# Performance work log

Hardware: AMD Instinct MI355X
Metric: run time of the kernel (lower is better)

The kernel has to match this reference:

```python
import jax, jax.numpy as jnp
import numpy as np
import math

DIM = 2048
N_HEADS = 16
HEAD_DIM = DIM // N_HEADS
B, S = 2, 2048
EPS = 1e-6


def rms_norm(x, w):
    return x * jax.lax.rsqrt(jnp.mean(x * x, axis=-1, keepdims=True) + EPS) * w


def rotate(x, cos, sin):
    x1, x2 = jnp.split(x, 2, axis=-1)
    rotated = jnp.concatenate((-x2, x1), axis=-1)
    return x * cos + rotated * sin


def setup_inputs() -> dict:
    key = jax.random.key(0)
    ks = jax.random.split(key, 16)
    half = HEAD_DIM // 2
    inv_freq = 1.0 / (10000.0 ** (jnp.arange(0, half, dtype=jnp.float32) / half))
    t = jnp.arange(S, dtype=jnp.float32)
    freqs = jnp.einsum('s,d->sd', t, inv_freq)
    emb = jnp.concatenate((freqs, freqs), axis=-1)  # [S, HEAD_DIM]
    cos = jnp.cos(emb)[None, None]  # [1,1,S,HEAD_DIM]
    sin = jnp.sin(emb)[None, None]
    # causal additive mask [1,1,S,S]
    causal = jnp.triu(jnp.full((S, S), -1e9, dtype=jnp.float32), k=1)[None, None]
    sc = 0.02
    return {
        'x': jax.random.normal(ks[0], (B, S, DIM), jnp.float32),
        'cos': cos,
        'sin': sin,
        'mask': causal,
        'attn_norm_w': jnp.ones((DIM,), jnp.float32),
        'ffn_norm_w': jnp.ones((DIM,), jnp.float32),
        'wq': jax.random.normal(ks[1], (DIM, DIM), jnp.float32) * sc,
        'wk': jax.random.normal(ks[2], (DIM, DIM), jnp.float32) * sc,
        'wv': jax.random.normal(ks[3], (DIM, DIM), jnp.float32) * sc,
        'wo': jax.random.normal(ks[4], (DIM, DIM), jnp.float32) * sc,
        'w1': jax.random.normal(ks[5], (DIM, 4 * DIM), jnp.float32) * sc,
        'w2': jax.random.normal(ks[6], (4 * DIM, DIM), jnp.float32) * sc,
        'w3': jax.random.normal(ks[7], (DIM, 4 * DIM), jnp.float32) * sc,
    }


def reference(x, cos, sin, mask, attn_norm_w, ffn_norm_w, wq, wk, wv, wo, w1, w2, w3):
    b, s, d = x.shape
    h = rms_norm(x, attn_norm_w)
    q = (h @ wq).reshape(b, s, N_HEADS, HEAD_DIM).transpose(0, 2, 1, 3)
    k = (h @ wk).reshape(b, s, N_HEADS, HEAD_DIM).transpose(0, 2, 1, 3)
    v = (h @ wv).reshape(b, s, N_HEADS, HEAD_DIM).transpose(0, 2, 1, 3)
    q = rotate(q, cos, sin)
    k = rotate(k, cos, sin)
    attn = jnp.einsum('bhqd,bhkd->bhqk', q, k) / math.sqrt(HEAD_DIM)
    attn = attn + mask
    attn = jax.nn.softmax(attn, axis=-1)
    out = jnp.einsum('bhqk,bhkd->bhqd', attn, v)
    out = out.transpose(0, 2, 1, 3).reshape(b, s, d)
    x = x + out @ wo
    h = rms_norm(x, ffn_norm_w)
    x = x + (jax.nn.silu(h @ w1) * (h @ w3)) @ w2
    return x
```

## Files before the change

kernel.cpp:

```cpp
#include <hip/hip_runtime.h>

#define DIM 2048
#define HDIM 128
#define NH 16
#define SEQ 2048
#define BATCH 2
#define MROWS (BATCH*SEQ)
#define QKP 6144

typedef __attribute__((ext_vector_type(8))) short short8;
typedef __attribute__((ext_vector_type(4))) float f32x4;

template<int N> struct ic { static constexpr int value = N; };

__device__ __forceinline__ unsigned short f2bf(float f) {
  union { float f; unsigned u; } v; v.f = f;
  unsigned r = v.u + 0x7FFFu + ((v.u >> 16) & 1u);
  return (unsigned short)(r >> 16);
}
__device__ __forceinline__ float bf2f(unsigned short b) {
  union { unsigned u; float f; } v; v.u = ((unsigned)b) << 16;
  return v.f;
}

__device__ __forceinline__ void gload16(const void* g, void* l) {
  __builtin_amdgcn_global_load_lds((const __attribute__((address_space(1))) unsigned int*)g,
                                   (__attribute__((address_space(3))) unsigned int*)l,
                                   16, 0, 0);
}

__global__ __launch_bounds__(256) void rmsnorm_kernel(const float* __restrict__ x,
                                                      const float* __restrict__ w,
                                                      unsigned short* __restrict__ out) {
  const int row = blockIdx.x;
  const int t = threadIdx.x;
  const float* xr = x + (size_t)row * DIM;
  float4 v0 = ((const float4*)xr)[t*2];
  float4 v1 = ((const float4*)xr)[t*2+1];
  float ss = v0.x*v0.x + v0.y*v0.y + v0.z*v0.z + v0.w*v0.w
           + v1.x*v1.x + v1.y*v1.y + v1.z*v1.z + v1.w*v1.w;
  #pragma unroll
  for (int i = 1; i < 64; i <<= 1) ss += __shfl_xor(ss, i);
  __shared__ float red[4];
  if ((t & 63) == 0) red[t >> 6] = ss;
  __syncthreads();
  float sum = red[0] + red[1] + red[2] + red[3];
  float sc = rsqrtf(sum * (1.0f/DIM) + 1e-6f);
  const float* wr = w + t*8;
  unsigned short ob[8];
  ob[0] = f2bf(v0.x*sc*wr[0]); ob[1] = f2bf(v0.y*sc*wr[1]);
  ob[2] = f2bf(v0.z*sc*wr[2]); ob[3] = f2bf(v0.w*sc*wr[3]);
  ob[4] = f2bf(v1.x*sc*wr[4]); ob[5] = f2bf(v1.y*sc*wr[5]);
  ob[6] = f2bf(v1.z*sc*wr[6]); ob[7] = f2bf(v1.w*sc*wr[7]);
  uint4 pk;
  pk.x = (unsigned)ob[0] | ((unsigned)ob[1] << 16);
  pk.y = (unsigned)ob[2] | ((unsigned)ob[3] << 16);
  pk.z = (unsigned)ob[4] | ((unsigned)ob[5] << 16);
  pk.w = (unsigned)ob[6] | ((unsigned)ob[7] << 16);
  *((uint4*)(out + (size_t)row*DIM + t*8)) = pk;
}

__global__ __launch_bounds__(256) void transpose3_kernel(const float* __restrict__ W0,
                                                         const float* __restrict__ W1,
                                                         const float* __restrict__ W2,
                                                         unsigned short* __restrict__ D0,
                                                         unsigned short* __restrict__ D1,
                                                         unsigned short* __restrict__ D2,
                                                         int K, int N) {
  const float* W = blockIdx.z == 0 ? W0 : (blockIdx.z == 1 ? W1 : W2);
  unsigned short* D = blockIdx.z == 0 ? D0 : (blockIdx.z == 1 ? D1 : D2);
  __shared__ float tile[64][65];
  const int k0 = blockIdx.x*64, n0 = blockIdx.y*64;
  const int t = threadIdx.x;
  const int rr = t >> 4, cc = (t & 15) * 4;
  #pragma unroll
  for (int i=0;i<4;i++) {
    float4 v = *(const float4*)&W[(size_t)(k0 + rr + i*16)*N + n0 + cc];
    tile[rr+i*16][cc] = v.x; tile[rr+i*16][cc+1] = v.y;
    tile[rr+i*16][cc+2] = v.z; tile[rr+i*16][cc+3] = v.w;
  }
  __syncthreads();
  #pragma unroll
  for (int j=0;j<4;j++) {
    const int n = rr + j*16;
    uint2 pk;
    pk.x = (unsigned)f2bf(tile[cc  ][n]) | ((unsigned)f2bf(tile[cc+1][n]) << 16);
    pk.y = (unsigned)f2bf(tile[cc+2][n]) | ((unsigned)f2bf(tile[cc+3][n]) << 16);
    *(uint2*)&D[(size_t)(n0 + n)*K + k0 + cc] = pk;
  }
}

__global__ __launch_bounds__(256) void transpose_v_kernel(const unsigned short* __restrict__ v,
                                                          int vpitch,
                                                          unsigned short* __restrict__ vt) {
  __shared__ unsigned short tile[32][33];
  const int b = blockIdx.z;
  const int s0 = blockIdx.x*32, c0 = blockIdx.y*32;
  const int tx = threadIdx.x & 31, ty = threadIdx.x >> 5;
  #pragma unroll
  for (int i=0;i<4;i++) tile[ty+i*8][tx] = v[((size_t)(b*SEQ + s0+ty+i*8))*vpitch + c0+tx];
  __syncthreads();
  #pragma unroll
  for (int i=0;i<4;i++) vt[((size_t)(b*DIM + c0+ty+i*8))*SEQ + s0+tx] = tile[tx][ty+i*8];
}

__global__ __launch_bounds__(256) void rope_qk(unsigned short* __restrict__ qk,
                                               const float* __restrict__ cosb,
                                               const float* __restrict__ sinb) {
  const size_t idx = (size_t)blockIdx.x * 256 + threadIdx.x;
  const int d = (int)(idx & 63);
  const int h = (int)((idx >> 6) & 31);
  const int row = (int)(idx >> 11);
  const int s = row & (SEQ-1);
  const size_t base = (size_t)row * QKP + h*HDIM + d;
  float a  = bf2f(qk[base]);
  float bq = bf2f(qk[base+64]);
  float c1 = cosb[s*HDIM + d],    s1 = sinb[s*HDIM + d];
  float c2 = cosb[s*HDIM + d+64], s2 = sinb[s*HDIM + d+64];
  qk[base]    = f2bf(a*c1 - bq*s1);
  qk[base+64] = f2bf(bq*c2 + a*s2);
}

template<int EPI>
__global__ __launch_bounds__(512, 2) void gemm_pipe32(const unsigned short* __restrict__ A,
                                                      const unsigned short* __restrict__ Bt,
                                                      const float* __restrict__ aux,
                                                      void* __restrict__ outp,
                                                      int M, int N, int K) {
  extern __shared__ unsigned short ldsd[];
  const int tid = threadIdx.x, l = tid & 63, wid = tid >> 6;
  const int wm = wid >> 2, wn = wid & 3;
  const int lr = l & 15, lg = l >> 4;
  const int bh = wn >> 1, brow0 = (wn & 1)*64;

  const int nbx = N >> 8;
  const int SW = (nbx >= 8) ? (nbx >> 3) : 1;
  const int xcd = (int)blockIdx.x & 7;
  const int ii  = (int)blockIdx.x >> 3;
  const int by = ii / SW;
  const int bx = xcd * SW + (ii % SW);
  const int m0 = by * 256, n0 = bx * 256;

  const int jks = ((lg ^ ((lr ^ (lr >> 2)) & 3)) << 3);
  const unsigned short* ldsA0 = ldsd + wm*4096 + lr*32 + jks;
  const unsigned short* ldsB0 = ldsd + 16384 + bh*4096 + brow0*32 + lr*32 + jks;

  const int srow = tid >> 2;
  const int jsw = (((tid & 3) ^ ((srow ^ (srow >> 2)) & 3)) << 3);
  const unsigned short* srcA[2];
  const unsigned short* srcB[2];
  #pragma unroll
  for (int h=0;h<2;h++) {
    srcA[h] = A  + (size_t)(m0 + h*128 + srow)*K + jsw;
    srcB[h] = Bt + (size_t)(n0 + h*128 + srow)*K + jsw;
  }
  unsigned short* dstL = ldsd + tid*8;

  int kO = 0;
  auto stA = [&](int db, int half, int tiled) {
    gload16(srcA[half] + kO + tiled, dstL + (db*2+half)*4096);
  };
  auto stB = [&](int db, int half, int tiled) {
    gload16(srcB[half] + kO + tiled, dstL + 16384 + (db*2+half)*4096);
  };

  f32x4 acc[8][4] = {};
  short8 bfrag[4];
  const int ntile = K >> 5;

  stB(0,0,0); stB(0,1,0);
  stA(0,0,0); stA(0,1,0);
  stB(1,0,32); stB(1,1,32);
  asm volatile("s_waitcnt vmcnt(2)" ::: "memory");
  __builtin_amdgcn_sched_barrier(0);
  __builtin_amdgcn_s_barrier();

  auto phase = [&](auto PC, auto LC) {
    constexpr int P = decltype(PC)::value;
    constexpr int LAST = decltype(LC)::value;
    constexpr int hi = P >> 2;
    constexpr int p  = P & 3;
    if constexpr (p == 0) {
      const unsigned short* bB = ldsB0 + hi*2*4096;
      #pragma unroll
      for (int nf=0;nf<4;nf++) bfrag[nf] = *(const short8*)(bB + nf*512);
    }
    const unsigned short* aB = ldsA0 + hi*2*4096;
    short8 afr[2];
    afr[0] = *(const short8*)(aB + (p*2  )*512);
    afr[1] = *(const short8*)(aB + (p*2+1)*512);
    if constexpr (P == 0)      stA(1, 0, 32);
    else if constexpr (P == 1) stA(1, 1, 32);
    else if constexpr (!LAST) {
      if constexpr (P == 2)      stB(0, 0, 64);
      else if constexpr (P == 3) stB(0, 1, 64);
      else if constexpr (P == 4) stA(0, 0, 64);
      else if constexpr (P == 5) stA(0, 1, 64);
      else if constexpr (P == 6) stB(1, 0, 96);
      else if constexpr (P == 7) stB(1, 1, 96);
    }
    if constexpr (P == 3) {
      if constexpr (LAST) { asm volatile("s_waitcnt vmcnt(0)" ::: "memory"); }
      else                { asm volatile("s_waitcnt vmcnt(2)" ::: "memory"); }
    }
    if constexpr (P == 7 && !LAST) {
      asm volatile("s_waitcnt vmcnt(2)" ::: "memory");
    }
    __builtin_amdgcn_s_barrier();
    asm volatile("s_waitcnt lgkmcnt(0)" ::: "memory");
    __builtin_amdgcn_sched_barrier(0);
    __builtin_amdgcn_s_setprio(1);
    #pragma unroll
    for (int mi=0;mi<2;mi++)
      #pragma unroll
      for (int nf=0;nf<4;nf++)
        acc[p*2+mi][nf] = __builtin_amdgcn_mfma_f32_16x16x32_bf16(afr[mi], bfrag[nf], acc[p*2+mi][nf], 0,0,0);
    __builtin_amdgcn_s_setprio(0);
    __builtin_amdgcn_s_barrier();
  };

  for (int T = 0; T + 2 < ntile; T += 2, kO += 64) {
    phase(ic<0>{}, ic<0>{}); phase(ic<1>{}, ic<0>{});
    phase(ic<2>{}, ic<0>{}); phase(ic<3>{}, ic<0>{});
    phase(ic<4>{}, ic<0>{}); phase(ic<5>{}, ic<0>{});
    phase(ic<6>{}, ic<0>{}); phase(ic<7>{}, ic<0>{});
  }
  phase(ic<0>{}, ic<1>{}); phase(ic<1>{}, ic<1>{});
  phase(ic<2>{}, ic<1>{}); phase(ic<3>{}, ic<1>{});
  phase(ic<4>{}, ic<1>{}); phase(ic<5>{}, ic<1>{});
  phase(ic<6>{}, ic<1>{}); phase(ic<7>{}, ic<1>{});

  #pragma unroll
  for (int mf = 0; mf < 8; mf++)
    #pragma unroll
    for (int nf = 0; nf < 4; nf++)
      #pragma unroll
      for (int r = 0; r < 4; r++) {
        const int row = m0 + wm*128 + mf*16 + lg*4 + r;
        const int col = n0 + wn*64 + nf*16 + lr;
        const size_t idx = (size_t)row * N + col;
        if constexpr (EPI == 0) {
          ((unsigned short*)outp)[idx] = f2bf(acc[mf][nf][r]);
        } else if constexpr (EPI == 1) {
          ((float*)outp)[idx] = acc[mf][nf][r] + aux[idx];
        } else {
          float g = acc[mf][nf][r];
          float u = bf2f(((unsigned short*)outp)[idx]);
          float sg = u / (1.0f + __expf(-u));
          ((unsigned short*)outp)[idx] = f2bf(sg * g);
        }
      }
}

template<int BM, int EPI>
__global__ __launch_bounds__(512, 2) void gemm_pipe(const unsigned short* __restrict__ A,
                                                    const unsigned short* __restrict__ Bt,
                                                    const float* __restrict__ aux,
                                                    void* __restrict__ outp,
                                                    int M, int N, int K) {
  constexpr int HRA = BM/2;
  constexpr int MF  = BM/32;
  constexpr int APP = MF/4;
  constexpr int LA  = BM/128;
  constexpr int AHS = HRA*64;
  constexpr int BB  = 4*AHS;
  extern __shared__ unsigned short ldsd[];
  const int tid = threadIdx.x, l = tid & 63, wid = tid >> 6;
  const int wm = wid >> 2, wn = wid & 3;
  const int lr = l & 15, lg = l >> 4;
  const int bh = wn >> 1, brow0 = (wn & 1)*64;

  const int nbx = N >> 8;
  const int SW = (nbx >= 8) ? (nbx >> 3) : 1;
  const int xcd = (int)blockIdx.x & 7;
  const int ii  = (int)blockIdx.x >> 3;
  const int by = ii / SW;
  const int bx = xcd * SW + (ii % SW);
  const int m0 = by * BM, n0 = bx * 256;

  const int m7 = lr & 7;
  const int jks0 = ((lg    ) ^ m7) << 3;
  const int jks1 = ((4 + lg) ^ m7) << 3;
  const unsigned short* ldsA0 = ldsd + wm*AHS + lr*64;
  const unsigned short* ldsA1 = ldsA0 + 2*AHS;
  const unsigned short* ldsB0 = ldsd + BB + bh*8192 + (brow0+lr)*64;
  const unsigned short* ldsB1 = ldsB0 + 2*8192;

  const int r0 = tid >> 3;
  const int jsw = ((tid & 7) ^ (r0 & 7)) << 3;
  const unsigned short* srcA[2][LA];
  #pragma unroll
  for (int h=0;h<2;h++)
    #pragma unroll
    for (int c=0;c<LA;c++)
      srcA[h][c] = A + (size_t)(m0 + h*HRA + c*64 + r0)*K + jsw;
  const unsigned short* srcB[2][2];
  #pragma unroll
  for (int h=0;h<2;h++)
    #pragma unroll
    for (int c=0;c<2;c++)
      srcB[h][c] = Bt + (size_t)(n0 + h*128 + c*64 + r0)*K + jsw;
  unsigned short* dstL = ldsd + tid*8;

  int kO = 0;
  auto stA = [&](int db, int half, int tiled) {
    #pragma unroll
    for (int c=0;c<LA;c++)
      gload16(srcA[half][c] + kO + tiled, dstL + (db*2+half)*AHS + c*4096);
  };
  auto stB = [&](int db, int half, int tiled) {
    #pragma unroll
    for (int c=0;c<2;c++)
      gload16(srcB[half][c] + kO + tiled, dstL + BB + (db*2+half)*8192 + c*4096);
  };

  f32x4 acc[MF][4] = {};
  short8 bfrag[4][2];
  const int ntile = K >> 6;

  stB(0,0,0); stB(0,1,0);
  stA(0,0,0); stA(0,1,0);
  stB(1,0,64); stB(1,1,64);
  asm volatile("s_waitcnt vmcnt(4)" ::: "memory");
  __builtin_amdgcn_sched_barrier(0);
  __builtin_amdgcn_s_barrier();

  auto phase = [&](auto PC, auto LC) {
    constexpr int P = decltype(PC)::value;
    constexpr int LAST = decltype(LC)::value;
    constexpr int hi = P >> 2;
    constexpr int p  = P & 3;
    if constexpr (p == 0) {
      const unsigned short* bB = hi ? ldsB1 : ldsB0;
      #pragma unroll
      for (int nf=0;nf<4;nf++) {
        bfrag[nf][0] = *(const short8*)(bB + nf*1024 + jks0);
        bfrag[nf][1] = *(const short8*)(bB + nf*1024 + jks1);
      }
    }
    const unsigned short* aB = hi ? ldsA1 : ldsA0;
    short8 afr[APP][2];
    #pragma unroll
    for (int mi=0;mi<APP;mi++) {
      afr[mi][0] = *(const short8*)(aB + (p*APP+mi)*1024 + jks0);
      afr[mi][1] = *(const short8*)(aB + (p*APP+mi)*1024 + jks1);
    }
    if constexpr (P == 0)      stA(1, 0, 64);
    else if constexpr (P == 1) stA(1, 1, 64);
    else if constexpr (!LAST) {
      if constexpr (P == 2)      stB(0, 0, 128);
      else if constexpr (P == 3) stB(0, 1, 128);
      else if constexpr (P == 4) stA(0, 0, 128);
      else if constexpr (P == 5) stA(0, 1, 128);
      else if constexpr (P == 6) stB(1, 0, 192);
      else if constexpr (P == 7) stB(1, 1, 192);
    }
    if constexpr (p == 0) {
      asm volatile("s_waitcnt lgkmcnt(8)" ::: "memory");
    }
    if constexpr (P == 3) {
      if constexpr (LAST) { asm volatile("s_waitcnt vmcnt(0)" ::: "memory"); }
      else                { asm volatile("s_waitcnt vmcnt(4)" ::: "memory"); }
    }
    if constexpr (P == 7 && !LAST) {
      asm volatile("s_waitcnt vmcnt(4)" ::: "memory");
    }
    __builtin_amdgcn_s_barrier();
    asm volatile("s_waitcnt lgkmcnt(0)" ::: "memory");
    __builtin_amdgcn_sched_barrier(0);
    __builtin_amdgcn_s_setprio(1);
    #pragma unroll
    for (int mi=0;mi<APP;mi++)
      #pragma unroll
      for (int nf=0;nf<4;nf++)
        #pragma unroll
        for (int ks=0;ks<2;ks++)
          acc[p*APP+mi][nf] = __builtin_amdgcn_mfma_f32_16x16x32_bf16(afr[mi][ks], bfrag[nf][ks], acc[p*APP+mi][nf], 0,0,0);
    __builtin_amdgcn_s_setprio(0);
    __builtin_amdgcn_s_barrier();
  };

  for (int T = 0; T + 2 < ntile; T += 2, kO += 128) {
    phase(ic<0>{}, ic<0>{}); phase(ic<1>{}, ic<0>{});
    phase(ic<2>{}, ic<0>{}); phase(ic<3>{}, ic<0>{});
    phase(ic<4>{}, ic<0>{}); phase(ic<5>{}, ic<0>{});
    phase(ic<6>{}, ic<0>{}); phase(ic<7>{}, ic<0>{});
  }
  phase(ic<0>{}, ic<1>{}); phase(ic<1>{}, ic<1>{});
  phase(ic<2>{}, ic<1>{}); phase(ic<3>{}, ic<1>{});
  phase(ic<4>{}, ic<1>{}); phase(ic<5>{}, ic<1>{});
  phase(ic<6>{}, ic<1>{}); phase(ic<7>{}, ic<1>{});

  #pragma unroll
  for (int mf = 0; mf < MF; mf++)
    #pragma unroll
    for (int nf = 0; nf < 4; nf++)
      #pragma unroll
      for (int r = 0; r < 4; r++) {
        const int row = m0 + wm*HRA + mf*16 + lg*4 + r;
        const int col = n0 + wn*64 + nf*16 + lr;
        const size_t idx = (size_t)row * N + col;
        if constexpr (EPI == 0) {
          ((unsigned short*)outp)[idx] = f2bf(acc[mf][nf][r]);
        } else if constexpr (EPI == 1) {
          ((float*)outp)[idx] = acc[mf][nf][r] + aux[idx];
        } else {
          float g = acc[mf][nf][r];
          float u = bf2f(((unsigned short*)outp)[idx]);
          float sg = u / (1.0f + __expf(-u));
          ((unsigned short*)outp)[idx] = f2bf(sg * g);
        }
      }
}

__global__ __launch_bounds__(256, 2) void attn_kernel(const unsigned short* __restrict__ q,
                                                      const unsigned short* __restrict__ k,
                                                      const unsigned short* __restrict__ vt,
                                                      unsigned short* __restrict__ ao) {
  const int t = threadIdx.x, lane = t & 63, w = t >> 6;
  const int qt = (int)gridDim.x - 1 - (int)blockIdx.x;
  const int bh = blockIdx.y;
  const int b = bh >> 4, h = bh & 15;
  const int lr = lane & 15, lg = lane >> 4;
  const int q0w = qt*128 + w*32;

  __shared__ __attribute__((aligned(16))) unsigned short Kb[64*128];
  __shared__ __attribute__((aligned(16))) unsigned short Vb[128*64];
  __shared__ __attribute__((aligned(16))) unsigned short Ones[16*72];
  __shared__ __attribute__((aligned(16))) unsigned short P[4][32*72];
  unsigned short* pw = &P[w][0];

  for (int idx = t; idx < 16*72; idx += 256) Ones[idx] = (idx < 72) ? 0x3F80 : 0;

  short8 aq[2][4];
  {
    const unsigned short* qp = q + ((size_t)(b*SEQ + q0w + lr))*QKP + h*HDIM;
    #pragma unroll
    for (int mf=0;mf<2;mf++)
      #pragma unroll
      for (int c=0;c<4;c++) aq[mf][c] = *(const short8*)(qp + (size_t)mf*16*QKP + c*32 + lg*8);
  }

  f32x4 accO[2][8] = {};
  f32x4 accO9[2] = {};
  float mrow[2][4];
  #pragma unroll
  for (int mf=0;mf<2;mf++)
    #pragma unroll
    for (int r=0;r<4;r++) mrow[mf][r] = -3.0e38f;

  const float scale = 0.08838834764831845f;
  const unsigned short* kg = k + (size_t)(b*SEQ)*QKP + h*HDIM;
  const unsigned short* vg = vt + (size_t)(bh*HDIM)*SEQ;

  const unsigned short* kga[4]; const unsigned short* vga[4];
  unsigned short* kld[4]; unsigned short* vld[4];
  #pragma unroll
  for (int i=0;i<4;i++) {
    const int D = i*256 + t;
    const int rk = D >> 4, jk = D & 15;
    kga[i] = kg + (size_t)rk*QKP + ((jk ^ (rk & 7)) * 8);
    const int rv = D >> 3, jv = D & 7;
    vga[i] = vg + (size_t)rv*SEQ + ((jv ^ (rv & 7)) * 8);
    kld[i] = &Kb[i*2048 + w*512];
    vld[i] = &Vb[i*2048 + w*512];
  }

  const int KV_END = qt*128 + 128;

  for (int kv0 = 0; kv0 < KV_END; kv0 += 64) {
    #pragma unroll
    for (int i=0;i<4;i++) gload16(kga[i] + (size_t)kv0*QKP, kld[i]);
    #pragma unroll
    for (int i=0;i<4;i++) gload16(vga[i] + kv0, vld[i]);
    __syncthreads();

    if (kv0 < q0w + 32) {
      f32x4 sc[2][4] = {};
      #pragma unroll
      for (int blk=0;blk<4;blk++) {
        const int krow = blk*16 + lr;
        const int sw = (krow & 7) << 3;
        #pragma unroll
        for (int c=0;c<4;c++) {
          short8 bk = *(const short8*)&Kb[krow*128 + ((c*32 + lg*8) ^ sw)];
          sc[0][blk] = __builtin_amdgcn_mfma_f32_16x16x32_bf16(aq[0][c], bk, sc[0][blk], 0,0,0);
          sc[1][blk] = __builtin_amdgcn_mfma_f32_16x16x32_bf16(aq[1][c], bk, sc[1][blk], 0,0,0);
        }
      }
      #pragma unroll
      for (int mf=0;mf<2;mf++)
        #pragma unroll
        for (int blk=0;blk<4;blk++)
          #pragma unroll
          for (int r=0;r<4;r++) sc[mf][blk][r] *= scale;
      if (kv0 + 63 > q0w) {
        #pragma unroll
        for (int mf=0;mf<2;mf++)
          #pragma unroll
          for (int blk=0;blk<4;blk++)
            #pragma unroll
            for (int r=0;r<4;r++)
              if (kv0 + blk*16 + lr > q0w + mf*16 + lg*4 + r) sc[mf][blk][r] = -1.0e30f;
      }
      float pm[2][4];
      #pragma unroll
      for (int mf=0;mf<2;mf++)
        #pragma unroll
        for (int r=0;r<4;r++) {
          float m0 = fmaxf(fmaxf(sc[mf][0][r], sc[mf][1][r]), fmaxf(sc[mf][2][r], sc[mf][3][r]));
          #pragma unroll
          for (int x=1;x<16;x<<=1) m0 = fmaxf(m0, __shfl_xor(m0, x));
          pm[mf][r] = m0;
        }
      int need = 0;
      #pragma unroll
      for (int mf=0;mf<2;mf++)
        #pragma unroll
        for (int r=0;r<4;r++) need |= (pm[mf][r] > mrow[mf][r] + 8.0f) ? 1 : 0;
      if (__any(need)) {
        #pragma unroll
        for (int mf=0;mf<2;mf++)
          #pragma unroll
          for (int r=0;r<4;r++) {
            const float mn = fmaxf(mrow[mf][r], pm[mf][r]);
            const float fc = __expf(mrow[mf][r] - mn);
            mrow[mf][r] = mn;
            #pragma unroll
            for (int n=0;n<8;n++) accO[mf][n][r] *= fc;
            accO9[mf][r] *= fc;
          }
      }
      #pragma unroll
      for (int mf=0;mf<2;mf++)
        #pragma unroll
        for (int blk=0;blk<4;blk++)
          #pragma unroll
          for (int r=0;r<4;r++) {
            const float p = __expf(sc[mf][blk][r] - mrow[mf][r]);
            pw[(mf*16 + lg*4 + r)*72 + blk*16 + lr] = f2bf(p);
          }
      short8 ap[2][2];
      #pragma unroll
      for (int mf=0;mf<2;mf++)
        #pragma unroll
        for (int ks=0;ks<2;ks++) ap[mf][ks] = *(const short8*)&pw[(mf*16 + lr)*72 + ks*32 + lg*8];
      #pragma unroll
      for (int n=0;n<8;n++) {
        #pragma unroll
        for (int ks=0;ks<2;ks++) {
          const int vrow = n*16 + lr;
          const int sw = (vrow & 7) << 3;
          short8 bv = *(const short8*)&Vb[vrow*64 + ((ks*32 + lg*8) ^ sw)];
          accO[0][n] = __builtin_amdgcn_mfma_f32_16x16x32_bf16(ap[0][ks], bv, accO[0][n], 0,0,0);
          accO[1][n] = __builtin_amdgcn_mfma_f32_16x16x32_bf16(ap[1][ks], bv, accO[1][n], 0,0,0);
        }
      }
      #pragma unroll
      for (int ks=0;ks<2;ks++) {
        short8 bv9 = *(const short8*)&Ones[lr*72 + ks*32 + lg*8];
        accO9[0] = __builtin_amdgcn_mfma_f32_16x16x32_bf16(ap[0][ks], bv9, accO9[0], 0,0,0);
        accO9[1] = __builtin_amdgcn_mfma_f32_16x16x32_bf16(ap[1][ks], bv9, accO9[1], 0,0,0);
      }
    }
    __syncthreads();
  }

  #pragma unroll
  for (int mf=0;mf<2;mf++)
    #pragma unroll
    for (int r=0;r<4;r++) {
      const float lv = __shfl(accO9[mf][r], lane & 48);
      const float inv = 1.0f / lv;
      const size_t row = (size_t)(b*SEQ + q0w + mf*16 + lg*4 + r);
      #pragma unroll
      for (int n=0;n<8;n++)
        ao[row*DIM + h*HDIM + n*16 + lr] = f2bf(accO[mf][n][r] * inv);
    }
}

extern "C" void kernel_launch(void* const* d_in, const int* in_sizes, int n_in,
                              void* d_out, int out_size, void* d_ws, size_t ws_size,
                              hipStream_t stream) {
  (void)in_sizes; (void)n_in; (void)out_size; (void)ws_size;
  const float* x    = (const float*)d_in[0];
  const float* cosb = (const float*)d_in[1];
  const float* sinb = (const float*)d_in[2];
  const float* anw  = (const float*)d_in[4];
  const float* fnw  = (const float*)d_in[5];
  const float* wq   = (const float*)d_in[6];
  const float* wk   = (const float*)d_in[7];
  const float* wv   = (const float*)d_in[8];
  const float* wo   = (const float*)d_in[9];
  const float* w1   = (const float*)d_in[10];
  const float* w2   = (const float*)d_in[11];
  const float* w3   = (const float*)d_in[12];

  char* ws = (char*)d_ws;
  const size_t MB = 1048576;
  unsigned short* h     = (unsigned short*)(ws);
  unsigned short* qkvb  = (unsigned short*)(ws + 16*MB);
  unsigned short* mid   = qkvb;
  unsigned short* aob   = (unsigned short*)(ws + 67*MB);
  char* wt              = ws + 84*MB;
  unsigned short* wqkvT = (unsigned short*)wt;
  unsigned short* vtb   = (unsigned short*)wt;
  unsigned short* woT   = (unsigned short*)wt;
  unsigned short* w1T   = (unsigned short*)wt;
  unsigned short* w3T   = (unsigned short*)(wt + 32*MB);
  unsigned short* w2T   = (unsigned short*)wt;
  float* x1f = (float*)d_out;

  dim3 b256(256);
  constexpr unsigned LDS32 = 65536;
  constexpr unsigned LDS128 = 98304;

  rmsnorm_kernel<<<dim3(MROWS), b256, 0, stream>>>(x, anw, h);

  transpose3_kernel<<<dim3(32,32,3), b256, 0, stream>>>(wq, wk, wv,
      wqkvT, wqkvT + 4194304, wqkvT + 8388608, 2048, 2048);

  gemm_pipe32<0><<<dim3(384), dim3(512), LDS32, stream>>>(h, wqkvT, nullptr, qkvb, MROWS, 6144, 2048);

  rope_qk<<<dim3(32768), b256, 0, stream>>>(qkvb, cosb, sinb);

  transpose_v_kernel<<<dim3(64,64,2), b256, 0, stream>>>(qkvb + 4096, QKP, vtb);

  attn_kernel<<<dim3(16,32), b256, 0, stream>>>(qkvb, qkvb + 2048, vtb, aob);

  transpose3_kernel<<<dim3(32,32,1), b256, 0, stream>>>(wo, nullptr, nullptr,
      woT, nullptr, nullptr, 2048, 2048);
  gemm_pipe<128,1><<<dim3(256), dim3(512), LDS128, stream>>>(aob, woT, x, x1f, MROWS, 2048, 2048);

  rmsnorm_kernel<<<dim3(MROWS), b256, 0, stream>>>(x1f, fnw, h);

  transpose3_kernel<<<dim3(32,128,2), b256, 0, stream>>>(w1, w3, nullptr,
      w1T, w3T, nullptr, 2048, 8192);
  gemm_pipe32<0><<<dim3(512), dim3(512), LDS32, stream>>>(h, w1T, nullptr, mid, MROWS, 8192, 2048);
  gemm_pipe32<3><<<dim3(512), dim3(512), LDS32, stream>>>(h, w3T, nullptr, mid, MROWS, 8192, 2048);

  transpose3_kernel<<<dim3(128,32,1), b256, 0, stream>>>(w2, nullptr, nullptr,
      w2T, nullptr, nullptr, 8192, 2048);
  gemm_pipe<128,1><<<dim3(256), dim3(512), LDS128, stream>>>(mid, w2T, x1f, (float*)d_out, MROWS, 2048, 8192);
}
```

Baseline: 850.9 us.

## Fuse W1/W3 FFN GEMMs into dual-B kernel and use BK64 GEMM for QKV

Replaces the two separate gate/up GEMMs with a single kernel that loads each A tile once and multiplies it against both W1 and W3 tiles, then applies SiLU-times-gate in registers before writing. This avoids a second pass over the activations and the bf16 round-trip of the intermediate gate output. The QKV projection also switches from the 32-wide-K kernel to the existing 128-row gemm_pipe variant with more blocks. The dual kernel needs 160 KB of LDS and two accumulator sets, which likely limits it to one block per CU and raises register pressure.

```diff
diff --git a/kernel.cpp b/kernel.cpp
--- a/kernel.cpp
+++ b/kernel.cpp
@@ -121,137 +121,6 @@
   qk[base+64] = f2bf(bq*c2 + a*s2);
 }
 
-template<int EPI>
-__global__ __launch_bounds__(512, 2) void gemm_pipe32(const unsigned short* __restrict__ A,
-                                                      const unsigned short* __restrict__ Bt,
-                                                      const float* __restrict__ aux,
-                                                      void* __restrict__ outp,
-                                                      int M, int N, int K) {
-  extern __shared__ unsigned short ldsd[];
-  const int tid = threadIdx.x, l = tid & 63, wid = tid >> 6;
-  const int wm = wid >> 2, wn = wid & 3;
-  const int lr = l & 15, lg = l >> 4;
-  const int bh = wn >> 1, brow0 = (wn & 1)*64;
-
-  const int nbx = N >> 8;
-  const int SW = (nbx >= 8) ? (nbx >> 3) : 1;
-  const int xcd = (int)blockIdx.x & 7;
-  const int ii  = (int)blockIdx.x >> 3;
-  const int by = ii / SW;
-  const int bx = xcd * SW + (ii % SW);
-  const int m0 = by * 256, n0 = bx * 256;
-
-  const int jks = ((lg ^ ((lr ^ (lr >> 2)) & 3)) << 3);
-  const unsigned short* ldsA0 = ldsd + wm*4096 + lr*32 + jks;
-  const unsigned short* ldsB0 = ldsd + 16384 + bh*4096 + brow0*32 + lr*32 + jks;
-
-  const int srow = tid >> 2;
-  const int jsw = (((tid & 3) ^ ((srow ^ (srow >> 2)) & 3)) << 3);
-  const unsigned short* srcA[2];
-  const unsigned short* srcB[2];
-  #pragma unroll
-  for (int h=0;h<2;h++) {
-    srcA[h] = A  + (size_t)(m0 + h*128 + srow)*K + jsw;
-    srcB[h] = Bt + (size_t)(n0 + h*128 + srow)*K + jsw;
-  }
-  unsigned short* dstL = ldsd + tid*8;
-
-  int kO = 0;
-  auto stA = [&](int db, int half, int tiled) {
-    gload16(srcA[half] + kO + tiled, dstL + (db*2+half)*4096);
-  };
-  auto stB = [&](int db, int half, int tiled) {
-    gload16(srcB[half] + kO + tiled, dstL + 16384 + (db*2+half)*4096);
-  };
-
-  f32x4 acc[8][4] = {};
-  short8 bfrag[4];
-  const int ntile = K >> 5;
-
-  stB(0,0,0); stB(0,1,0);
-  stA(0,0,0); stA(0,1,0);
-  stB(1,0,32); stB(1,1,32);
-  asm volatile("s_waitcnt vmcnt(2)" ::: "memory");
-  __builtin_amdgcn_sched_barrier(0);
-  __builtin_amdgcn_s_barrier();
-
-  auto phase = [&](auto PC, auto LC) {
-    constexpr int P = decltype(PC)::value;
-    constexpr int LAST = decltype(LC)::value;
-    constexpr int hi = P >> 2;
-    constexpr int p  = P & 3;
-    if constexpr (p == 0) {
-      const unsigned short* bB = ldsB0 + hi*2*4096;
-      #pragma unroll
-      for (int nf=0;nf<4;nf++) bfrag[nf] = *(const short8*)(bB + nf*512);
-    }
-    const unsigned short* aB = ldsA0 + hi*2*4096;
-    short8 afr[2];
-    afr[0] = *(const short8*)(aB + (p*2  )*512);
-    afr[1] = *(const short8*)(aB + (p*2+1)*512);
-    if constexpr (P == 0)      stA(1, 0, 32);
-    else if constexpr (P == 1) stA(1, 1, 32);
-    else if constexpr (!LAST) {
-      if constexpr (P == 2)      stB(0, 0, 64);
-      else if constexpr (P == 3) stB(0, 1, 64);
-      else if constexpr (P == 4) stA(0, 0, 64);
-      else if constexpr (P == 5) stA(0, 1, 64);
-      else if constexpr (P == 6) stB(1, 0, 96);
-      else if constexpr (P == 7) stB(1, 1, 96);
-    }
-    if constexpr (P == 3) {
-      if constexpr (LAST) { asm volatile("s_waitcnt vmcnt(0)" ::: "memory"); }
-      else                { asm volatile("s_waitcnt vmcnt(2)" ::: "memory"); }
-    }
-    if constexpr (P == 7 && !LAST) {
-      asm volatile("s_waitcnt vmcnt(2)" ::: "memory");
-    }
-    __builtin_amdgcn_s_barrier();
-    asm volatile("s_waitcnt lgkmcnt(0)" ::: "memory");
-    __builtin_amdgcn_sched_barrier(0);
-    __builtin_amdgcn_s_setprio(1);
-    #pragma unroll
-    for (int mi=0;mi<2;mi++)
-      #pragma unroll
-      for (int nf=0;nf<4;nf++)
-        acc[p*2+mi][nf] = __builtin_amdgcn_mfma_f32_16x16x32_bf16(afr[mi], bfrag[nf], acc[p*2+mi][nf], 0,0,0);
-    __builtin_amdgcn_s_setprio(0);
-    __builtin_amdgcn_s_barrier();
-  };
-
-  for (int T = 0; T + 2 < ntile; T += 2, kO += 64) {
-    phase(ic<0>{}, ic<0>{}); phase(ic<1>{}, ic<0>{});
-    phase(ic<2>{}, ic<0>{}); phase(ic<3>{}, ic<0>{});
-    phase(ic<4>{}, ic<0>{}); phase(ic<5>{}, ic<0>{});
-    phase(ic<6>{}, ic<0>{}); phase(ic<7>{}, ic<0>{});
-  }
-  phase(ic<0>{}, ic<1>{}); phase(ic<1>{}, ic<1>{});
-  phase(ic<2>{}, ic<1>{}); phase(ic<3>{}, ic<1>{});
-  phase(ic<4>{}, ic<1>{}); phase(ic<5>{}, ic<1>{});
-  phase(ic<6>{}, ic<1>{}); phase(ic<7>{}, ic<1>{});
-
-  #pragma unroll
-  for (int mf = 0; mf < 8; mf++)
-    #pragma unroll
-    for (int nf = 0; nf < 4; nf++)
-      #pragma unroll
-      for (int r = 0; r < 4; r++) {
-        const int row = m0 + wm*128 + mf*16 + lg*4 + r;
-        const int col = n0 + wn*64 + nf*16 + lr;
-        const size_t idx = (size_t)row * N + col;
-        if constexpr (EPI == 0) {
-          ((unsigned short*)outp)[idx] = f2bf(acc[mf][nf][r]);
-        } else if constexpr (EPI == 1) {
-          ((float*)outp)[idx] = acc[mf][nf][r] + aux[idx];
-        } else {
-          float g = acc[mf][nf][r];
-          float u = bf2f(((unsigned short*)outp)[idx]);
-          float sg = u / (1.0f + __expf(-u));
-          ((unsigned short*)outp)[idx] = f2bf(sg * g);
-        }
-      }
-}
-
 template<int BM, int EPI>
 __global__ __launch_bounds__(512, 2) void gemm_pipe(const unsigned short* __restrict__ A,
                                                     const unsigned short* __restrict__ Bt,
@@ -413,6 +282,157 @@
       }
 }
 
+__global__ __launch_bounds__(512, 2) void gemm_dual(const unsigned short* __restrict__ A,
+                                                    const unsigned short* __restrict__ B1t,
+                                                    const unsigned short* __restrict__ B3t,
+                                                    unsigned short* __restrict__ outp,
+                                                    int M, int N, int K) {
+  constexpr int AHS = 4096;
+  constexpr int BB1 = 16384;
+  constexpr int BB3 = 49152;
+  extern __shared__ unsigned short ldsd[];
+  const int tid = threadIdx.x, l = tid & 63, wid = tid >> 6;
+  const int wm = wid >> 2, wn = wid & 3;
+  const int lr = l & 15, lg = l >> 4;
+  const int bh = wn >> 1, brow0 = (wn & 1)*64;
+
+  const int nbx = N >> 8;
+  const int SW = nbx >> 3;
+  const int xcd = (int)blockIdx.x & 7;
+  const int ii  = (int)blockIdx.x >> 3;
+  const int by = ii / SW;
+  const int bx = xcd * SW + (ii % SW);
+  const int m0 = by * 128, n0 = bx * 256;
+
+  const int m7 = lr & 7;
+  const int jks0 = ((lg    ) ^ m7) << 3;
+  const int jks1 = ((4 + lg) ^ m7) << 3;
+  const unsigned short* ldsA0 = ldsd + wm*AHS + lr*64;
+  const unsigned short* ldsB1_ = ldsd + BB1 + bh*8192 + (brow0+lr)*64;
+  const unsigned short* ldsB3_ = ldsd + BB3 + bh*8192 + (brow0+lr)*64;
+
+  const int r0 = tid >> 3;
+  const int jsw = ((tid & 7) ^ (r0 & 7)) << 3;
+  const unsigned short* srcA[2];
+  #pragma unroll
+  for (int h=0;h<2;h++) srcA[h] = A + (size_t)(m0 + h*64 + r0)*K + jsw;
+  const unsigned short* srcB1[2][2];
+  const unsigned short* srcB3[2][2];
+  #pragma unroll
+  for (int h=0;h<2;h++)
+    #pragma unroll
+    for (int c=0;c<2;c++) {
+      srcB1[h][c] = B1t + (size_t)(n0 + h*128 + c*64 + r0)*K + jsw;
+      srcB3[h][c] = B3t + (size_t)(n0 + h*128 + c*64 + r0)*K + jsw;
+    }
+  unsigned short* dstL = ldsd + tid*8;
+
+  int kO = 0;
+  auto stA = [&](int db, int half, int tiled) {
+    gload16(srcA[half] + kO + tiled, dstL + (db*2+half)*AHS);
+  };
+  auto stBB = [&](int db, int half, int tiled) {
+    #pragma unroll
+    for (int c=0;c<2;c++)
+      gload16(srcB1[half][c] + kO + tiled, dstL + BB1 + (db*2+half)*8192 + c*4096);
+    #pragma unroll
+    for (int c=0;c<2;c++)
+      gload16(srcB3[half][c] + kO + tiled, dstL + BB3 + (db*2+half)*8192 + c*4096);
+  };
+
+  f32x4 acc1[4][4] = {};
+  f32x4 acc3[4][4] = {};
+  short8 bf1[4][2], bf3[4][2];
+  const int ntile = K >> 6;
+
+  stBB(0,0,0); stBB(0,1,0);
+  stA(0,0,0); stA(0,1,0);
+  stBB(1,0,64); stBB(1,1,64);
+  asm volatile("s_waitcnt vmcnt(8)" ::: "memory");
+  __builtin_amdgcn_sched_barrier(0);
+  __builtin_amdgcn_s_barrier();
+
+  auto phase = [&](auto PC, auto LC) {
+    constexpr int P = decltype(PC)::value;
+    constexpr int LAST = decltype(LC)::value;
+    constexpr int hi = P >> 2;
+    constexpr int p  = P & 3;
+    if constexpr (p == 0) {
+      const unsigned short* b1 = ldsB1_ + hi*2*8192;
+      const unsigned short* b3 = ldsB3_ + hi*2*8192;
+      #pragma unroll
+      for (int nf=0;nf<4;nf++) {
+        bf1[nf][0] = *(const short8*)(b1 + nf*1024 + jks0);
+        bf1[nf][1] = *(const short8*)(b1 + nf*1024 + jks1);
+        bf3[nf][0] = *(const short8*)(b3 + nf*1024 + jks0);
+        bf3[nf][1] = *(const short8*)(b3 + nf*1024 + jks1);
+      }
+    }
+    const unsigned short* aB = ldsA0 + hi*2*AHS;
+    short8 afr[2];
+    afr[0] = *(const short8*)(aB + p*1024 + jks0);
+    afr[1] = *(const short8*)(aB + p*1024 + jks1);
+    if constexpr (P == 0)      stA(1, 0, 64);
+    else if constexpr (P == 1) stA(1, 1, 64);
+    else if constexpr (!LAST) {
+      if constexpr (P == 2)      stBB(0, 0, 128);
+      else if constexpr (P == 3) stBB(0, 1, 128);
+      else if constexpr (P == 4) stA(0, 0, 128);
+      else if constexpr (P == 5) stA(0, 1, 128);
+      else if constexpr (P == 6) stBB(1, 0, 192);
+      else if constexpr (P == 7) stBB(1, 1, 192);
+    }
+    if constexpr (p == 0) {
+      asm volatile("s_waitcnt lgkmcnt(15)" ::: "memory");
+    }
+    if constexpr (P == 3) {
+      if constexpr (LAST) { asm volatile("s_waitcnt vmcnt(0)" ::: "memory"); }
+      else                { asm volatile("s_waitcnt vmcnt(8)" ::: "memory"); }
+    }
+    if constexpr (P == 7 && !LAST) {
+      asm volatile("s_waitcnt vmcnt(8)" ::: "memory");
+    }
+    __builtin_amdgcn_s_barrier();
+    asm volatile("s_waitcnt lgkmcnt(0)" ::: "memory");
+    __builtin_amdgcn_sched_barrier(0);
+    __builtin_amdgcn_s_setprio(1);
+    #pragma unroll
+    for (int nf=0;nf<4;nf++)
+      #pragma unroll
+      for (int ks=0;ks<2;ks++) {
+        acc1[p][nf] = __builtin_amdgcn_mfma_f32_16x16x32_bf16(afr[ks], bf1[nf][ks], acc1[p][nf], 0,0,0);
+        acc3[p][nf] = __builtin_amdgcn_mfma_f32_16x16x32_bf16(afr[ks], bf3[nf][ks], acc3[p][nf], 0,0,0);
+      }
+    __builtin_amdgcn_s_setprio(0);
+    __builtin_amdgcn_s_barrier();
+  };
+
+  for (int T = 0; T + 2 < ntile; T += 2, kO += 128) {
+    phase(ic<0>{}, ic<0>{}); phase(ic<1>{}, ic<0>{});
+    phase(ic<2>{}, ic<0>{}); phase(ic<3>{}, ic<0>{});
+    phase(ic<4>{}, ic<0>{}); phase(ic<5>{}, ic<0>{});
+    phase(ic<6>{}, ic<0>{}); phase(ic<7>{}, ic<0>{});
+  }
+  phase(ic<0>{}, ic<1>{}); phase(ic<1>{}, ic<1>{});
+  phase(ic<2>{}, ic<1>{}); phase(ic<3>{}, ic<1>{});
+  phase(ic<4>{}, ic<1>{}); phase(ic<5>{}, ic<1>{});
+  phase(ic<6>{}, ic<1>{}); phase(ic<7>{}, ic<1>{});
+
+  #pragma unroll
+  for (int mf = 0; mf < 4; mf++)
+    #pragma unroll
+    for (int nf = 0; nf < 4; nf++)
+      #pragma unroll
+      for (int r = 0; r < 4; r++) {
+        const int row = m0 + wm*64 + mf*16 + lg*4 + r;
+        const int col = n0 + wn*64 + nf*16 + lr;
+        const float u = acc1[mf][nf][r];
+        const float g = acc3[mf][nf][r];
+        const float sg = u / (1.0f + __expf(-u));
+        outp[(size_t)row * N + col] = f2bf(sg * g);
+      }
+}
+
 __global__ __launch_bounds__(256, 2) void attn_kernel(const unsigned short* __restrict__ q,
                                                       const unsigned short* __restrict__ k,
                                                       const unsigned short* __restrict__ vt,
@@ -612,15 +632,15 @@
   float* x1f = (float*)d_out;
 
   dim3 b256(256);
-  constexpr unsigned LDS32 = 65536;
   constexpr unsigned LDS128 = 98304;
+  constexpr unsigned LDSDUAL = 163840;
 
   rmsnorm_kernel<<<dim3(MROWS), b256, 0, stream>>>(x, anw, h);
 
   transpose3_kernel<<<dim3(32,32,3), b256, 0, stream>>>(wq, wk, wv,
       wqkvT, wqkvT + 4194304, wqkvT + 8388608, 2048, 2048);
 
-  gemm_pipe32<0><<<dim3(384), dim3(512), LDS32, stream>>>(h, wqkvT, nullptr, qkvb, MROWS, 6144, 2048);
+  gemm_pipe<128,0><<<dim3(768), dim3(512), LDS128, stream>>>(h, wqkvT, nullptr, qkvb, MROWS, 6144, 2048);
 
   rope_qk<<<dim3(32768), b256, 0, stream>>>(qkvb, cosb, sinb);
 
@@ -636,8 +656,7 @@
 
   transpose3_kernel<<<dim3(32,128,2), b256, 0, stream>>>(w1, w3, nullptr,
       w1T, w3T, nullptr, 2048, 8192);
-  gemm_pipe32<0><<<dim3(512), dim3(512), LDS32, stream>>>(h, w1T, nullptr, mid, MROWS, 8192, 2048);
-  gemm_pipe32<3><<<dim3(512), dim3(512), LDS32, stream>>>(h, w3T, nullptr, mid, MROWS, 8192, 2048);
+  gemm_dual<<<dim3(1024), dim3(512), LDSDUAL, stream>>>(h, w1T, w3T, mid, MROWS, 8192, 2048);
 
   transpose3_kernel<<<dim3(128,32,1), b256, 0, stream>>>(w2, nullptr, nullptr,
       w2T, nullptr, nullptr, 8192, 2048);
```

After: 921.5 us. 1.08x slower.
